# Kernel optimization log

Hardware: AMD Instinct MI355X
Metric: run time of the kernel (lower is better)

Reference implementation:

```python
import jax, jax.numpy as jnp
import numpy as np
import math

B, S, E = 1, 1024, 2880          # batch, seq, hidden_size
H, KV, D = 64, 8, 64             # query heads, kv heads, head_dim
WIN = 128                        # sliding window
BASE, SCALE, ORIG = 150000.0, 32.0, 4096
BFAST, BSLOW = 32.0, 1.0
SCALING = D ** -0.5
NEG = jnp.finfo(jnp.float32).min


def _rope_tables(positions):
    """YaRN-scaled RoPE cos/sin tables, matching RotaryEmbedding._build_cache."""
    def find_dim(rot):
        return D * math.log(ORIG / (rot * 2 * math.pi)) / (2 * math.log(BASE))
    low = max(find_dim(BFAST), 0.0)
    high = min(find_dim(BSLOW), D // 2 - 1)
    if low == high:
        high += 0.001
    pos_freqs = BASE ** (jnp.arange(0, D, 2, dtype=jnp.float32) / D)
    ramp = jnp.clip((jnp.arange(D // 2, dtype=jnp.float32) - low) / (high - low), 0.0, 1.0)
    inv_freq = (1.0 / (SCALE * pos_freqs)) * ramp + (1.0 / pos_freqs) * (1.0 - ramp)
    mscale = 0.1 * math.log(SCALE) + 1.0
    ang = positions.astype(jnp.float32)[:, None] * inv_freq[None, :]   # [S, D/2]
    emb = jnp.concatenate([ang, ang], axis=-1)                          # [S, D]
    return jnp.cos(emb) * mscale, jnp.sin(emb) * mscale


def _apply_rope(x, cos, sin):
    # x: [B, S, h, D]; cos/sin: [S, D]
    c = cos[None, :, None, :]
    s = sin[None, :, None, :]
    half = D // 2
    rot = jnp.concatenate([-x[..., half:], x[..., :half]], axis=-1)
    return x * c + rot * s


def setup_inputs() -> dict:
    key = jax.random.key(0)
    ks = jax.random.split(key, 10)
    std = 0.02
    return {
        "hidden_states": jax.random.normal(ks[0], (B, S, E), jnp.float32),
        "positions": jnp.arange(S, dtype=jnp.int32),
        "Wq": jax.random.normal(ks[1], (H * D, E), jnp.float32) * std,
        "bq": jax.random.normal(ks[2], (H * D,), jnp.float32) * std,
        "Wk": jax.random.normal(ks[3], (KV * D, E), jnp.float32) * std,
        "bk": jax.random.normal(ks[4], (KV * D,), jnp.float32) * std,
        "Wv": jax.random.normal(ks[5], (KV * D, E), jnp.float32) * std,
        "bv": jax.random.normal(ks[6], (KV * D,), jnp.float32) * std,
        "Wo": jax.random.normal(ks[7], (E, H * D), jnp.float32) * std,
        "bo": jax.random.normal(ks[8], (E,), jnp.float32) * std,
        "sinks": jax.random.normal(ks[9], (H,), jnp.float32) * 0.5,
    }


def reference(hidden_states, positions, Wq, bq, Wk, bk, Wv, bv, Wo, bo, sinks):
    x = hidden_states
    q = (x @ Wq.T + bq).reshape(B, S, H, D)
    k = (x @ Wk.T + bk).reshape(B, S, KV, D)
    v = (x @ Wv.T + bv).reshape(B, S, KV, D)

    cos, sin = _rope_tables(positions)
    q = _apply_rope(q, cos, sin)
    k = _apply_rope(k, cos, sin)

    rep = H // KV  # GQA: each kv head serves 8 query heads
    k = jnp.repeat(k, rep, axis=2)  # [B, S, H, D]
    v = jnp.repeat(v, rep, axis=2)

    scores = jnp.einsum("bqhd,bkhd->bhqk", q, k) * SCALING  # [B, H, S, S]
    i = jnp.arange(S)
    allowed = (i[None, :] <= i[:, None]) & (i[:, None] - i[None, :] < WIN)  # causal + window
    scores = jnp.where(allowed[None, None], scores, NEG)

    # learned per-head sink logit joins the softmax denominator
    sink = jnp.broadcast_to(sinks[None, :, None, None], (B, H, S, 1))
    probs = jax.nn.softmax(jnp.concatenate([scores, sink], axis=-1), axis=-1)[..., :-1]

    out = jnp.einsum("bhqk,bkhd->bqhd", probs, v).reshape(B, S, H * D)
    return out @ Wo.T + bo
```

## Files before the change

### kernel.cpp

```cpp
#include <hip/hip_runtime.h>
#include <math.h>

#define S_LEN 1024
#define QKV_N 5120

typedef __attribute__((ext_vector_type(8))) __bf16 bf16x8;
typedef __attribute__((ext_vector_type(4))) float f32x4;

__device__ __forceinline__ unsigned short f2bf(float f) {
  unsigned int u = __float_as_uint(f);
  u += 0x7fff + ((u >> 16) & 1);
  return (unsigned short)(u >> 16);
}
__device__ __forceinline__ float bf2f(unsigned short u) {
  return __uint_as_float((unsigned int)u << 16);
}

__device__ __forceinline__ void async_copy16(const void* g, void* l) {
  __builtin_amdgcn_global_load_lds(
      (const __attribute__((address_space(1))) unsigned int*)g,
      (__attribute__((address_space(3))) unsigned int*)l, 16, 0, 0);
}

__global__ void prep_all(const float* __restrict__ x, const float* __restrict__ Wq,
                         const float* __restrict__ Wk, const float* __restrict__ Wv,
                         const float* __restrict__ Wo, const float* __restrict__ bq,
                         const float* __restrict__ bk, const float* __restrict__ bv,
                         const int* __restrict__ positions,
                         unsigned short* __restrict__ xb, unsigned short* __restrict__ wqkv,
                         unsigned short* __restrict__ wo, float* __restrict__ bqkv,
                         float* __restrict__ cosT, float* __restrict__ sinT,
                         float low, float high, float mscale) {
  int i = blockIdx.x * 256 + threadIdx.x;
  if (i < 7372800) {
    const float* src;
    unsigned short* dst;
    int off;
    if (i < 737280)       { src = x;  dst = xb;                          off = i; }
    else if (i < 3686400) { src = Wq; dst = wqkv;                        off = i - 737280; }
    else if (i < 4055040) { src = Wk; dst = wqkv + (size_t)4096 * 2880;  off = i - 3686400; }
    else if (i < 4423680) { src = Wv; dst = wqkv + (size_t)4608 * 2880;  off = i - 4055040; }
    else                  { src = Wo; dst = wo;                          off = i - 4423680; }
    float4 v = ((const float4*)src)[off];
    ushort4 r;
    r.x = f2bf(v.x); r.y = f2bf(v.y); r.z = f2bf(v.z); r.w = f2bf(v.w);
    ((ushort4*)dst)[off] = r;
  } else if (i < 7374080) {
    int b = i - 7372800;
    int c0 = b * 4;
    float4 v;
    if (c0 < 4096)      v = ((const float4*)bq)[b];
    else if (c0 < 4608) v = ((const float4*)bk)[b - 1024];
    else                v = ((const float4*)bv)[b - 1152];
    ((float4*)bqkv)[b] = v;
  } else if (i < 7382272) {
    int tid = i - 7374080;
    int s = tid >> 3;
    int j0 = (tid & 7) * 4;
    float pos = (float)positions[s];
    float4 cv, sv;
    float* cc = (float*)&cv;
    float* ss = (float*)&sv;
#pragma unroll
    for (int e = 0; e < 4; e++) {
      int j = j0 + e;
      float pf = powf(150000.0f, (float)j / 32.0f);
      float ramp = ((float)j - low) / (high - low);
      ramp = fminf(fmaxf(ramp, 0.0f), 1.0f);
      float invf = (1.0f / (32.0f * pf)) * ramp + (1.0f / pf) * (1.0f - ramp);
      float ang = pos * invf;
      cc[e] = cosf(ang) * mscale;
      ss[e] = sinf(ang) * mscale;
    }
    ((float4*)cosT)[s * 8 + (tid & 7)] = cv;
    ((float4*)sinT)[s * 8 + (tid & 7)] = sv;
  }
}

__global__ __launch_bounds__(256) void rope_vtrans(
    const unsigned short* __restrict__ part, const float* __restrict__ bqkv,
    const float* __restrict__ cosT, const float* __restrict__ sinT,
    unsigned short* __restrict__ Qb, unsigned short* __restrict__ Kb,
    unsigned short* __restrict__ Vt, int SP) {
  const int bx = blockIdx.x;
  const int t = threadIdx.x;
  __shared__ unsigned short tile[128][66];
  if (bx < 9216) {
    int idx = bx * 256 + t;
    int j = idx & 31;
    int hh = (idx >> 5) % 72;
    int s = idx / (72 * 32);
    int c1 = hh * 64 + j, c2 = c1 + 32;
    float xv = bqkv[c1], yv = bqkv[c2];
    for (int sp = 0; sp < SP; sp++) {
      const unsigned short* P = part + (size_t)sp * S_LEN * QKV_N + (size_t)s * QKV_N;
      xv += bf2f(P[c1]);
      yv += bf2f(P[c2]);
    }
    float c = cosT[s * 32 + j], sn = sinT[s * 32 + j];
    float o1 = xv * c - yv * sn;
    float o2 = yv * c + xv * sn;
    if (hh < 64) {
      unsigned short* q = Qb + ((size_t)s * 64 + hh) * 64;
      q[j]      = f2bf(o1 * 0.125f);
      q[j + 32] = f2bf(o2 * 0.125f);
    } else {
      unsigned short* k = Kb + ((size_t)s * 8 + (hh - 64)) * 64;
      k[j]      = f2bf(o1);
      k[j + 32] = f2bf(o2);
    }
  } else {
    const int b = bx - 9216;
    const int kvh = b >> 3, s0 = (b & 7) * 128;
#pragma unroll
    for (int i = 0; i < 32; i++) {
      int e = t + i * 256;
      int s = e >> 6, d = e & 63;
      int col = 4608 + kvh * 64 + d;
      float v = bqkv[col];
      for (int sp = 0; sp < SP; sp++)
        v += bf2f(part[(size_t)sp * S_LEN * QKV_N + (size_t)(s0 + s) * QKV_N + col]);
      tile[s][d] = f2bf(v);
    }
    __syncthreads();
#pragma unroll
    for (int i = 0; i < 32; i++) {
      int e = t + i * 256;
      int d = e >> 7, s = e & 127;
      Vt[((size_t)kvh * 64 + d) * 1024 + s0 + s] = tile[s][d];
    }
  }
}

__global__ __launch_bounds__(256) void gemm_bt_sk(
    const unsigned short* __restrict__ A, const unsigned short* __restrict__ B,
    unsigned short* __restrict__ part, int M, int N, int K, int NT, int SP) {
  __shared__ __align__(16) unsigned short As[128 * 64];
  __shared__ __align__(16) unsigned short Bs[128 * 64];
  const int lb = blockIdx.x;
  const int aI = lb >> 6;
  const int rem = lb & 63;
  const int mI = rem >> 3;
  const int bI = rem & 7;
  const int c = aI * 8 + bI;
  if (c >= NT * SP) return;
  const int sI = c / NT, nI = c % NT;
  const int m0 = mI * 128, n0 = nI * 128;

  const int t = threadIdx.x;
  const int l = t & 63;
  const int w = t >> 6;
  const int lr = l & 15, lq = l >> 4;
  const int wm = (w >> 1) * 64, wn = (w & 1) * 64;

  const int T = K >> 6;
  const int kb = ((sI * T) / SP) * 64;
  const int ke = (((sI + 1) * T) / SP) * 64;

  const unsigned short* gA[4];
  const unsigned short* gB[4];
  unsigned short* lA[4];
  unsigned short* lB[4];
#pragma unroll
  for (int q = 0; q < 4; q++) {
    int s = q * 256 + t;
    int row = s >> 3;
    int kgX = s & 7;
    int kg = kgX ^ (row & 7);
    gA[q] = A + (size_t)(m0 + row) * K + kg * 8;
    int rb = n0 + row; if (rb > N - 1) rb = N - 1;
    gB[q] = B + (size_t)rb * K + kg * 8;
    lA[q] = &As[s * 8];
    lB[q] = &Bs[s * 8];
  }

  f32x4 acc[4][4] = {};

  for (int k0 = kb; k0 < ke; k0 += 64) {
#pragma unroll
    for (int q = 0; q < 4; q++) async_copy16(gA[q] + k0, lA[q]);
#pragma unroll
    for (int q = 0; q < 4; q++) async_copy16(gB[q] + k0, lB[q]);
    __syncthreads();
#pragma unroll
    for (int h = 0; h < 2; h++) {
      bf16x8 af[4], bf[4];
#pragma unroll
      for (int i = 0; i < 4; i++) {
        int row = wm + i * 16 + lr;
        af[i] = *(const bf16x8*)&As[row * 64 + (((h << 2) | lq) ^ (row & 7)) * 8];
      }
#pragma unroll
      for (int i = 0; i < 4; i++) {
        int row = wn + i * 16 + lr;
        bf[i] = *(const bf16x8*)&Bs[row * 64 + (((h << 2) | lq) ^ (row & 7)) * 8];
      }
#pragma unroll
      for (int mi = 0; mi < 4; mi++)
#pragma unroll
        for (int ni = 0; ni < 4; ni++)
          acc[mi][ni] = __builtin_amdgcn_mfma_f32_16x16x32_bf16(af[mi], bf[ni], acc[mi][ni], 0, 0, 0);
    }
    __syncthreads();
  }

  unsigned short* P = part + (size_t)sI * M * N;
#pragma unroll
  for (int mi = 0; mi < 4; mi++) {
#pragma unroll
    for (int ni = 0; ni < 4; ni++) {
      int col = n0 + wn + ni * 16 + lr;
      if (col < N) {
#pragma unroll
        for (int r = 0; r < 4; r++) {
          int row = m0 + wm + mi * 16 + lq * 4 + r;
          P[(size_t)row * N + col] = f2bf(acc[mi][ni][r]);
        }
      }
    }
  }
}

__global__ void reduce_f32(const unsigned short* __restrict__ part, const float* __restrict__ bias,
                           float* __restrict__ out, int SP) {
  int i = blockIdx.x * 256 + threadIdx.x;
  if (i >= 368640) return;
  float acc[8];
  int bc = (i % 360) * 8;
#pragma unroll
  for (int e = 0; e < 8; e++) acc[e] = bias[bc + e];
  for (int sp = 0; sp < SP; sp++) {
    const ushort4* P = (const ushort4*)(part + (size_t)sp * 2949120);
    ushort4 u0 = P[i * 2], u1 = P[i * 2 + 1];
    acc[0] += bf2f(u0.x); acc[1] += bf2f(u0.y); acc[2] += bf2f(u0.z); acc[3] += bf2f(u0.w);
    acc[4] += bf2f(u1.x); acc[5] += bf2f(u1.y); acc[6] += bf2f(u1.z); acc[7] += bf2f(u1.w);
  }
  float4 o0 = {acc[0], acc[1], acc[2], acc[3]};
  float4 o1 = {acc[4], acc[5], acc[6], acc[7]};
  ((float4*)out)[i * 2] = o0;
  ((float4*)out)[i * 2 + 1] = o1;
}

__global__ __launch_bounds__(64) void attn_mfma(
    const unsigned short* __restrict__ Qb,
    const unsigned short* __restrict__ Kb,
    const unsigned short* __restrict__ Vt,
    const float* __restrict__ sinks,
    unsigned short* __restrict__ out) {
  const int h = blockIdx.x;
  const int q0 = blockIdx.y * 16;
  const int kvh = h >> 3;
  const int l = threadIdx.x;
  const int n = l & 15;
  const int g = l >> 4;

  __shared__ __align__(16) unsigned short Pl[16][32];

  const unsigned short* qp = Qb + (((size_t)(q0 + n) * 64 + h) * 64 + g * 8);
  bf16x8 qf0 = *(const bf16x8*)qp;
  bf16x8 qf1 = *(const bf16x8*)(qp + 32);

  const int q_lane = q0 + n;
  int k_lo = q0 - 127; if (k_lo < 0) k_lo = 0;
  k_lo &= ~31;
  const int k_end = q0 + 16;

  float m = -3.0e38f, lsum = 0.0f;
  f32x4 oacc[4] = {};

  for (int kk = k_lo; kk < k_end; kk += 32) {
    int kr0 = kk + n;      if (kr0 > 1023) kr0 = 1023;
    int kr1 = kk + 16 + n; if (kr1 > 1023) kr1 = 1023;
    const unsigned short* kp0 = Kb + (((size_t)kr0 * 8 + kvh) * 64 + g * 8);
    const unsigned short* kp1 = Kb + (((size_t)kr1 * 8 + kvh) * 64 + g * 8);
    bf16x8 ka0 = *(const bf16x8*)kp0;
    bf16x8 ka1 = *(const bf16x8*)(kp0 + 32);
    bf16x8 kb0 = *(const bf16x8*)kp1;
    bf16x8 kb1 = *(const bf16x8*)(kp1 + 32);
    f32x4 st0 = {}, st1 = {};
    st0 = __builtin_amdgcn_mfma_f32_16x16x32_bf16(ka0, qf0, st0, 0, 0, 0);
    st0 = __builtin_amdgcn_mfma_f32_16x16x32_bf16(ka1, qf1, st0, 0, 0, 0);
    st1 = __builtin_amdgcn_mfma_f32_16x16x32_bf16(kb0, qf0, st1, 0, 0, 0);
    st1 = __builtin_amdgcn_mfma_f32_16x16x32_bf16(kb1, qf1, st1, 0, 0, 0);

    float tm = -3.0e38f;
#pragma unroll
    for (int r = 0; r < 4; r++) {
      int k0i = kk + 4 * g + r;
      int k1i = k0i + 16;
      bool ok0 = (k0i <= q_lane) && (q_lane - k0i < 128);
      bool ok1 = (k1i <= q_lane) && (q_lane - k1i < 128);
      st0[r] = ok0 ? st0[r] : -3.0e38f;
      st1[r] = ok1 ? st1[r] : -3.0e38f;
      tm = fmaxf(tm, fmaxf(st0[r], st1[r]));
    }
    tm = fmaxf(tm, __shfl_xor(tm, 16));
    tm = fmaxf(tm, __shfl_xor(tm, 32));

    float mn = fmaxf(m, tm);
    float corr = __expf(m - mn);
    m = mn;
    float p0[4], p1[4], ps = 0.0f;
#pragma unroll
    for (int r = 0; r < 4; r++) {
      p0[r] = __expf(st0[r] - mn);
      p1[r] = __expf(st1[r] - mn);
      ps += p0[r] + p1[r];
    }
    ps += __shfl_xor(ps, 16);
    ps += __shfl_xor(ps, 32);
    lsum = lsum * corr + ps;

    ushort4 w0, w1;
    w0.x = f2bf(p0[0]); w0.y = f2bf(p0[1]); w0.z = f2bf(p0[2]); w0.w = f2bf(p0[3]);
    w1.x = f2bf(p1[0]); w1.y = f2bf(p1[1]); w1.z = f2bf(p1[2]); w1.w = f2bf(p1[3]);
    *(ushort4*)&Pl[n][4 * g]      = w0;
    *(ushort4*)&Pl[n][16 + 4 * g] = w1;
    __syncthreads();
    bf16x8 pf = *(const bf16x8*)&Pl[n][8 * g];
    __syncthreads();

#pragma unroll
    for (int db = 0; db < 4; db++) {
      const unsigned short* vp = Vt + ((size_t)(kvh * 64 + db * 16 + n)) * 1024 + kk + 8 * g;
      bf16x8 vf = *(const bf16x8*)vp;
#pragma unroll
      for (int r = 0; r < 4; r++) oacc[db][r] *= corr;
      oacc[db] = __builtin_amdgcn_mfma_f32_16x16x32_bf16(vf, pf, oacc[db], 0, 0, 0);
    }
  }

  float sink = sinks[h];
  float mn2 = fmaxf(m, sink);
  float corr2 = __expf(m - mn2);
  float denom = lsum * corr2 + __expf(sink - mn2);
  float fs = corr2 / denom;

#pragma unroll
  for (int db = 0; db < 4; db++) {
    ushort4 r;
    r.x = f2bf(oacc[db][0] * fs);
    r.y = f2bf(oacc[db][1] * fs);
    r.z = f2bf(oacc[db][2] * fs);
    r.w = f2bf(oacc[db][3] * fs);
    *(ushort4*)(out + (size_t)q_lane * 4096 + h * 64 + db * 16 + 4 * g) = r;
  }
}

extern "C" void kernel_launch(void* const* d_in, const int* in_sizes, int n_in,
                              void* d_out, int out_size, void* d_ws, size_t ws_size,
                              hipStream_t stream) {
  const float* x = (const float*)d_in[0];
  const int* positions = (const int*)d_in[1];
  const float* Wq = (const float*)d_in[2];
  const float* bq = (const float*)d_in[3];
  const float* Wk = (const float*)d_in[4];
  const float* bk = (const float*)d_in[5];
  const float* Wv = (const float*)d_in[6];
  const float* bv = (const float*)d_in[7];
  const float* Wo = (const float*)d_in[8];
  const float* bo = (const float*)d_in[9];
  const float* sinks = (const float*)d_in[10];
  float* out = (float*)d_out;

  char* ws = (char*)d_ws;
  unsigned short* xb   = (unsigned short*)(ws + 0);
  unsigned short* wqkv = (unsigned short*)(ws + 5898240);
  unsigned short* wo   = (unsigned short*)(ws + 35389440);
  float* bqkv          = (float*)(ws + 58982400);
  float* cosT          = (float*)(ws + 59002880);
  float* sinT          = (float*)(ws + 59133952);
  const size_t SH = 59265024;
  unsigned short* qkv_part = (unsigned short*)(ws + SH);
  unsigned short* out_part = (unsigned short*)(ws + SH);
  unsigned short* attnb    = (unsigned short*)(ws + SH + 23592960);
  const size_t TL = SH + 41943040;
  unsigned short* Qb = (unsigned short*)(ws + TL);
  unsigned short* Kb = (unsigned short*)(ws + TL + 8388608);
  unsigned short* Vt = (unsigned short*)(ws + TL + 9437184);

  int split_q = 4, split_o = 4;
  if (ws_size < TL + 10485888) {
    split_q = 2; split_o = 2;
    attnb = (unsigned short*)(ws + SH + 11796480);
    Qb = (unsigned short*)(ws + SH + 20971520);
    Kb = Qb + 4194304;
    Vt = Kb + 524288;
  }

  const double TWO_PI = 6.283185307179586;
  double lowd = 64.0 * log(4096.0 / (32.0 * TWO_PI)) / (2.0 * log(150000.0));
  if (lowd < 0.0) lowd = 0.0;
  double highd = 64.0 * log(4096.0 / (1.0 * TWO_PI)) / (2.0 * log(150000.0));
  if (highd > 31.0) highd = 31.0;
  if (lowd == highd) highd += 0.001;
  float mscale = (float)(0.1 * log(32.0) + 1.0);

  prep_all<<<28837, 256, 0, stream>>>(x, Wq, Wk, Wv, Wo, bq, bk, bv, positions,
                                      xb, wqkv, wo, bqkv, cosT, sinT,
                                      (float)lowd, (float)highd, mscale);

  {
    int NT = 40, C = NT * split_q;
    int grid = 64 * ((C + 7) / 8);
    gemm_bt_sk<<<grid, 256, 0, stream>>>(xb, wqkv, qkv_part, 1024, 5120, 2880, NT, split_q);
  }

  rope_vtrans<<<9280, 256, 0, stream>>>(qkv_part, bqkv, cosT, sinT, Qb, Kb, Vt, split_q);

  attn_mfma<<<dim3(64, 64), 64, 0, stream>>>(Qb, Kb, Vt, sinks, attnb);

  {
    int NT = 23, C = NT * split_o;
    int grid = 64 * ((C + 7) / 8);
    gemm_bt_sk<<<grid, 256, 0, stream>>>(attnb, wo, out_part, 1024, 2880, 4096, NT, split_o);
  }

  reduce_f32<<<1440, 256, 0, stream>>>(out_part, bo, out, split_o);
}
```

Measured before the change: 306.3 us.

## Fuse fp32-to-bf16 conversion of activations and weights into GEMM tile loads

Drops the standalone conversion pass that turned x, Wq/Wk/Wv and Wo into bf16 copies in workspace. The GEMMs now read fp32 directly, convert in registers and store bf16 into LDS, with the B operand chosen per row from three weight pointers. This removes one full read and write of about 29.5M weight elements, but the GEMM inner loop now uses synchronous global loads with twice the bytes instead of async global-to-LDS copies. Each weight tile is also loaded and converted once per M block, and there are 8 M blocks.

```diff
diff --git a/kernel.cpp b/kernel.cpp
--- a/kernel.cpp
+++ b/kernel.cpp
@@ -22,39 +22,27 @@
       (__attribute__((address_space(3))) unsigned int*)l, 16, 0, 0);
 }
 
-__global__ void prep_all(const float* __restrict__ x, const float* __restrict__ Wq,
-                         const float* __restrict__ Wk, const float* __restrict__ Wv,
-                         const float* __restrict__ Wo, const float* __restrict__ bq,
-                         const float* __restrict__ bk, const float* __restrict__ bv,
-                         const int* __restrict__ positions,
-                         unsigned short* __restrict__ xb, unsigned short* __restrict__ wqkv,
-                         unsigned short* __restrict__ wo, float* __restrict__ bqkv,
-                         float* __restrict__ cosT, float* __restrict__ sinT,
-                         float low, float high, float mscale) {
+__device__ __forceinline__ void cvt_store8(unsigned short* dst, float4 u0, float4 u1) {
+  bf16x8 v;
+  v[0] = (__bf16)u0.x; v[1] = (__bf16)u0.y; v[2] = (__bf16)u0.z; v[3] = (__bf16)u0.w;
+  v[4] = (__bf16)u1.x; v[5] = (__bf16)u1.y; v[6] = (__bf16)u1.z; v[7] = (__bf16)u1.w;
+  *(bf16x8*)dst = v;
+}
+
+__global__ void prep_small(const float* __restrict__ bq, const float* __restrict__ bk,
+                           const float* __restrict__ bv, const int* __restrict__ positions,
+                           float* __restrict__ bqkv, float* __restrict__ cosT,
+                           float* __restrict__ sinT, float low, float high, float mscale) {
   int i = blockIdx.x * 256 + threadIdx.x;
-  if (i < 7372800) {
-    const float* src;
-    unsigned short* dst;
-    int off;
-    if (i < 737280)       { src = x;  dst = xb;                          off = i; }
-    else if (i < 3686400) { src = Wq; dst = wqkv;                        off = i - 737280; }
-    else if (i < 4055040) { src = Wk; dst = wqkv + (size_t)4096 * 2880;  off = i - 3686400; }
-    else if (i < 4423680) { src = Wv; dst = wqkv + (size_t)4608 * 2880;  off = i - 4055040; }
-    else                  { src = Wo; dst = wo;                          off = i - 4423680; }
-    float4 v = ((const float4*)src)[off];
-    ushort4 r;
-    r.x = f2bf(v.x); r.y = f2bf(v.y); r.z = f2bf(v.z); r.w = f2bf(v.w);
-    ((ushort4*)dst)[off] = r;
-  } else if (i < 7374080) {
-    int b = i - 7372800;
-    int c0 = b * 4;
+  if (i < 1280) {
+    int c0 = i * 4;
     float4 v;
-    if (c0 < 4096)      v = ((const float4*)bq)[b];
-    else if (c0 < 4608) v = ((const float4*)bk)[b - 1024];
-    else                v = ((const float4*)bv)[b - 1152];
-    ((float4*)bqkv)[b] = v;
-  } else if (i < 7382272) {
-    int tid = i - 7374080;
+    if (c0 < 4096)      v = ((const float4*)bq)[i];
+    else if (c0 < 4608) v = ((const float4*)bk)[i - 1024];
+    else                v = ((const float4*)bv)[i - 1152];
+    ((float4*)bqkv)[i] = v;
+  } else if (i < 9472) {
+    int tid = i - 1280;
     int s = tid >> 3;
     int j0 = (tid & 7) * 4;
     float pos = (float)positions[s];
@@ -132,8 +120,11 @@
   }
 }
 
-__global__ __launch_bounds__(256) void gemm_bt_sk(
-    const unsigned short* __restrict__ A, const unsigned short* __restrict__ B,
+template <bool A_BF16>
+__global__ __launch_bounds__(256) void gemm_fused(
+    const void* __restrict__ Av, const float* __restrict__ B0,
+    const float* __restrict__ B1, const float* __restrict__ B2,
+    int b1row, int b2row,
     unsigned short* __restrict__ part, int M, int N, int K, int NT, int SP) {
   __shared__ __align__(16) unsigned short As[128 * 64];
   __shared__ __align__(16) unsigned short Bs[128 * 64];
@@ -158,29 +149,48 @@
   const int ke = (((sI + 1) * T) / SP) * 64;
 
   const unsigned short* gA[4];
-  const unsigned short* gB[4];
+  const float* gA32[4];
+  const float* gB32[4];
   unsigned short* lA[4];
   unsigned short* lB[4];
 #pragma unroll
   for (int q = 0; q < 4; q++) {
     int s = q * 256 + t;
     int row = s >> 3;
-    int kgX = s & 7;
-    int kg = kgX ^ (row & 7);
-    gA[q] = A + (size_t)(m0 + row) * K + kg * 8;
+    int kg = (s & 7) ^ (row & 7);
+    if (A_BF16)
+      gA[q] = (const unsigned short*)Av + (size_t)(m0 + row) * K + kg * 8;
+    else
+      gA32[q] = (const float*)Av + (size_t)(m0 + row) * K + kg * 8;
+    lA[q] = &As[s * 8];
     int rb = n0 + row; if (rb > N - 1) rb = N - 1;
-    gB[q] = B + (size_t)rb * K + kg * 8;
-    lA[q] = &As[s * 8];
+    const float* bb = (rb < b1row) ? B0 + (size_t)rb * K
+                     : (rb < b2row) ? B1 + (size_t)(rb - b1row) * K
+                                    : B2 + (size_t)(rb - b2row) * K;
+    gB32[q] = bb + kg * 8;
     lB[q] = &Bs[s * 8];
   }
 
   f32x4 acc[4][4] = {};
 
   for (int k0 = kb; k0 < ke; k0 += 64) {
-#pragma unroll
-    for (int q = 0; q < 4; q++) async_copy16(gA[q] + k0, lA[q]);
-#pragma unroll
-    for (int q = 0; q < 4; q++) async_copy16(gB[q] + k0, lB[q]);
+    if (A_BF16) {
+#pragma unroll
+      for (int q = 0; q < 4; q++) async_copy16(gA[q] + k0, lA[q]);
+    } else {
+#pragma unroll
+      for (int q = 0; q < 4; q++) {
+        float4 u0 = *(const float4*)(gA32[q] + k0);
+        float4 u1 = *(const float4*)(gA32[q] + k0 + 4);
+        cvt_store8(lA[q], u0, u1);
+      }
+    }
+#pragma unroll
+    for (int q = 0; q < 4; q++) {
+      float4 u0 = *(const float4*)(gB32[q] + k0);
+      float4 u1 = *(const float4*)(gB32[q] + k0 + 4);
+      cvt_store8(lB[q], u0, u1);
+    }
     __syncthreads();
 #pragma unroll
     for (int h = 0; h < 2; h++) {
@@ -364,13 +374,10 @@
   float* out = (float*)d_out;
 
   char* ws = (char*)d_ws;
-  unsigned short* xb   = (unsigned short*)(ws + 0);
-  unsigned short* wqkv = (unsigned short*)(ws + 5898240);
-  unsigned short* wo   = (unsigned short*)(ws + 35389440);
-  float* bqkv          = (float*)(ws + 58982400);
-  float* cosT          = (float*)(ws + 59002880);
-  float* sinT          = (float*)(ws + 59133952);
-  const size_t SH = 59265024;
+  float* bqkv = (float*)(ws + 0);
+  float* cosT = (float*)(ws + 20480);
+  float* sinT = (float*)(ws + 151552);
+  const size_t SH = 282624;
   unsigned short* qkv_part = (unsigned short*)(ws + SH);
   unsigned short* out_part = (unsigned short*)(ws + SH);
   unsigned short* attnb    = (unsigned short*)(ws + SH + 23592960);
@@ -380,7 +387,7 @@
   unsigned short* Vt = (unsigned short*)(ws + TL + 9437184);
 
   int split_q = 4, split_o = 4;
-  if (ws_size < TL + 10485888) {
+  if (ws_size < TL + 10489984) {
     split_q = 2; split_o = 2;
     attnb = (unsigned short*)(ws + SH + 11796480);
     Qb = (unsigned short*)(ws + SH + 20971520);
@@ -396,14 +403,14 @@
   if (lowd == highd) highd += 0.001;
   float mscale = (float)(0.1 * log(32.0) + 1.0);
 
-  prep_all<<<28837, 256, 0, stream>>>(x, Wq, Wk, Wv, Wo, bq, bk, bv, positions,
-                                      xb, wqkv, wo, bqkv, cosT, sinT,
-                                      (float)lowd, (float)highd, mscale);
+  prep_small<<<37, 256, 0, stream>>>(bq, bk, bv, positions, bqkv, cosT, sinT,
+                                     (float)lowd, (float)highd, mscale);
 
   {
     int NT = 40, C = NT * split_q;
     int grid = 64 * ((C + 7) / 8);
-    gemm_bt_sk<<<grid, 256, 0, stream>>>(xb, wqkv, qkv_part, 1024, 5120, 2880, NT, split_q);
+    gemm_fused<false><<<grid, 256, 0, stream>>>(x, Wq, Wk, Wv, 4096, 4608,
+                                                qkv_part, 1024, 5120, 2880, NT, split_q);
   }
 
   rope_vtrans<<<9280, 256, 0, stream>>>(qkv_part, bqkv, cosT, sinT, Qb, Kb, Vt, split_q);
@@ -413,7 +420,8 @@
   {
     int NT = 23, C = NT * split_o;
     int grid = 64 * ((C + 7) / 8);
-    gemm_bt_sk<<<grid, 256, 0, stream>>>(attnb, wo, out_part, 1024, 2880, 4096, NT, split_o);
+    gemm_fused<true><<<grid, 256, 0, stream>>>(attnb, Wo, Wo, Wo, 1 << 30, 1 << 30,
+                                               out_part, 1024, 2880, 4096, NT, split_o);
   }
 
   reduce_f32<<<1440, 256, 0, stream>>>(out_part, bo, out, split_o);
```

After: 347.6 us. 1.13x slower.
